# Optimization experiments

Measured on AMD Instinct MI355X. Metric: run time of the kernel, lower is better.

Reference implementation:

```python
import jax, jax.numpy as jnp
from jax import lax
import numpy as np

H = 16        # hidden_size == input_size
L = 8         # num_layers


def _lstm_layer(x_seq, Wih, Whh, bih, bhh):
    # x_seq: [B, T, H] -> outputs [B, T, H]; PyTorch gate order i,f,g,o
    B = x_seq.shape[0]
    b = bih + bhh  # [4H]

    def step(carry, xt):
        h, c = carry
        gates = xt @ Wih.T + h @ Whh.T + b  # [B, 4H]
        i, f, g, o = jnp.split(gates, 4, axis=-1)
        c = jax.nn.sigmoid(f) * c + jax.nn.sigmoid(i) * jnp.tanh(g)
        h = jax.nn.sigmoid(o) * jnp.tanh(c)
        return (h, c), h

    h0 = jnp.zeros((B, H), x_seq.dtype)
    (_, _), hs = lax.scan(step, (h0, h0), jnp.swapaxes(x_seq, 0, 1))
    return jnp.swapaxes(hs, 0, 1)  # [B, T, H]


def setup_inputs() -> dict:
    key = jax.random.key(0)
    ks = jax.random.split(key, 9)
    s = 1.0 / np.sqrt(H)  # PyTorch default init scale
    x = jax.random.normal(ks[0], (2048, 512, H), dtype=jnp.float32)
    W_ih = jax.random.uniform(ks[1], (L, 4 * H, H), jnp.float32, -s, s)
    W_hh = jax.random.uniform(ks[2], (L, 4 * H, H), jnp.float32, -s, s)
    b_ih = jax.random.uniform(ks[3], (L, 4 * H), jnp.float32, -s, s)
    b_hh = jax.random.uniform(ks[4], (L, 4 * H), jnp.float32, -s, s)
    Wp = jax.random.uniform(ks[5], (3, H), jnp.float32, -s, s)
    bp = jax.random.uniform(ks[6], (3,), jnp.float32, -s, s)
    Wo = jax.random.uniform(ks[7], (3, H), jnp.float32, -s, s)
    bo = jax.random.uniform(ks[8], (3,), jnp.float32, -s, s)
    return {"x": x, "W_ih": W_ih, "W_hh": W_hh, "b_ih": b_ih, "b_hh": b_hh,
            "Wp": Wp, "bp": bp, "Wo": Wo, "bo": bo}


def reference(x, W_ih, W_hh, b_ih, b_hh, Wp, bp, Wo, bo):
    h = x
    for l in range(L):  # fixed small layer count
        h = _lstm_layer(h, W_ih[l], W_hh[l], b_ih[l], b_hh[l])
    last = h[:, -1, :]                       # [B, H]
    position = last @ Wp.T + bp              # [B, 3]
    orientation = jnp.tanh(last @ Wo.T + bo) # [B, 3]
    return jnp.concatenate((position, orientation), axis=1)  # [B, 6]
```

## Files before the change

kernel.cpp:

```cpp
#include <hip/hip_runtime.h>
#include <math.h>

typedef _Float16 f16x8 __attribute__((ext_vector_type(8)));
typedef float    f32x4 __attribute__((ext_vector_type(4)));

constexpr int kT    = 512;
constexpr int kH    = 16;
constexpr int kL    = 8;
constexpr int kG    = 64;
constexpr int kNB   = 8;
constexpr int kPad  = 24;
constexpr int kRows = 9;
constexpr int kSlots= 16;
constexpr int kLyr  = kL + 1;
constexpr int kSE   = kLyr * kRows * kPad;
constexpr int kIters= 33;

constexpr float kL2E = 1.4426950408889634f;

__device__ __forceinline__ float sigm2(float z) {
    return __builtin_amdgcn_rcpf(1.0f + __builtin_amdgcn_exp2f(z));
}
__device__ __forceinline__ void cbar() { asm volatile("" ::: "memory"); }

__global__ __launch_bounds__(512, 2)
void lstm_rp(const float* __restrict__ x,
             const float* __restrict__ Wih, const float* __restrict__ Whh,
             const float* __restrict__ bih, const float* __restrict__ bhh,
             const float* __restrict__ Wp,  const float* __restrict__ bpos,
             const float* __restrict__ Wo,  const float* __restrict__ bori,
             float* __restrict__ out)
{
    const int tid  = threadIdx.x;
    const int l    = tid >> 6;
    const int lane = tid & 63;
    const int n    = lane & 15;
    const int q    = lane >> 4;
    const int bn   = n & 7;
    const bool cLow = (n < 8);
    const bool bact = ((q >> 1) == (n >> 3));

    __shared__ __align__(16) _Float16 hb[kSlots][kLyr][kRows][kPad];
    __shared__ int cnt[kL];

    {
        int* hz = (int*)&hb[0][0][0][0];
        for (int i = tid; i < (int)(sizeof(hb) / 4); i += 512) hz[i] = 0;
        if (tid < kL) cnt[tid] = -1;
    }

    auto loadA = [&](const float* W, int tile) -> f16x8 {
        const int unit = tile + (n >> 2) + ((q >= 2) ? 4 : 0);
        const int row  = (n & 3) * 16 + unit;
        const float* src = W + (size_t)l * kG * kH + row * kH + (q & 1) * 8;
        f16x8 a;
        #pragma unroll
        for (int j = 0; j < 8; ++j) a[j] = (_Float16)src[j];
        return a;
    };
    const f16x8 A1P1 = loadA(Wih, 0), A2P1 = loadA(Whh, 0);
    const f16x8 A1P2 = loadA(Wih, 8), A2P2 = loadA(Whh, 8);

    const int u1 = (cLow ? q : 4 + q);
    float ab1[4], ab2[4];
    #pragma unroll
    for (int r = 0; r < 4; ++r) {
        const float sc = (r == 2) ? (-2.0f * kL2E) : (-kL2E);
        const int g1 = l * kG + r * 16 + u1;
        const int g2 = l * kG + r * 16 + u1 + 8;
        ab1[r] = sc * (bih[g1] + bhh[g1]);
        ab2[r] = sc * (bih[g2] + bhh[g2]);
    }

    const int boff = (bact ? bn * kPad : 8 * kPad) + (q & 1) * 8;
    const _Float16* b1b = &hb[0][l    ][0][0] + boff;
    const _Float16* b2b = &hb[0][l + 1][0][0] + boff;
    _Float16* hw1 = &hb[0][l + 1][bn][u1];
    _Float16* hw2 = &hb[0][l + 1][bn][u1 + 8];
    _Float16* xwb = &hb[0][0][lane >> 3][(lane & 7) * 2];

    const float* xg_ptr =
        x + ((size_t)(blockIdx.x * kNB + (lane >> 3)) * kT) * kH + (lane & 7) * 2;
    float xg0 = 0.f, xg1 = 0.f;
    if (l == 0) {
        float2 v0 = *(const float2*)(xg_ptr);
        hb[15][0][lane >> 3][(lane & 7) * 2]     = (_Float16)v0.x;
        hb[15][0][lane >> 3][(lane & 7) * 2 + 1] = (_Float16)v0.y;
        float2 v1 = *(const float2*)(xg_ptr + kH);
        xg0 = v1.x; xg1 = v1.y;
    }

    float c1 = 0.f, c2 = 0.f;
    __syncthreads();

    const f32x4 zeroC = {0.f, 0.f, 0.f, 0.f};
    volatile const int* upc = (l > 0)      ? &cnt[l - 1] : nullptr;
    volatile const int* dnc = (l < kL - 1) ? &cnt[l + 1] : nullptr;

    for (int it = 0; it < kIters; ++it) {
        const int sb = it * 16;
        #pragma unroll
        for (int k = 0; k < 16; ++k) {
            const int s = sb + k;

            if ((k & 1) == 0 && l > 0) {
                while (*upc < s) __builtin_amdgcn_s_sleep(1);
                cbar();
            }
            if ((k == 0 || k == 8) && l < kL - 1) {
                const int need = (k == 0) ? (sb - 8) : sb;
                while (*dnc < need) __builtin_amdgcn_s_sleep(1);
                cbar();
            }

            const int  t      = s - l;
            const bool active = ((unsigned)t < (unsigned)kT);
            const int  rs     = (k + 15) & 15;
            const int  roff   = rs * kSE;
            const int  woff   = k * kSE;

            const f16x8 B1 = *(const f16x8*)(b1b + roff);
            const f16x8 B2 = *(const f16x8*)(b2b + roff);

            f32x4 d1 = __builtin_amdgcn_mfma_f32_16x16x32_f16(A2P1, B2, zeroC, 0, 0, 0);
            f32x4 d2 = __builtin_amdgcn_mfma_f32_16x16x32_f16(A2P2, B2, zeroC, 0, 0, 0);
            d1 = __builtin_amdgcn_mfma_f32_16x16x32_f16(A1P1, B1, d1, 0, 0, 0);
            d2 = __builtin_amdgcn_mfma_f32_16x16x32_f16(A1P2, B1, d2, 0, 0, 0);

            {
                const float iv = sigm2(fmaf(-kL2E,        d1[0], ab1[0]));
                const float fv = sigm2(fmaf(-kL2E,        d1[1], ab1[1]));
                const float gv = fmaf(2.f, sigm2(fmaf(-2.f * kL2E, d1[2], ab1[2])), -1.f);
                const float ov = sigm2(fmaf(-kL2E,        d1[3], ab1[3]));
                float cn = fmaf(fv, c1, iv * gv);
                cn = active ? cn : 0.0f;
                c1 = cn;
                const float tc = fmaf(2.f, sigm2(-2.f * kL2E * cn), -1.f);
                hw1[woff] = (_Float16)(ov * tc);
            }
            {
                const float iv = sigm2(fmaf(-kL2E,        d2[0], ab2[0]));
                const float fv = sigm2(fmaf(-kL2E,        d2[1], ab2[1]));
                const float gv = fmaf(2.f, sigm2(fmaf(-2.f * kL2E, d2[2], ab2[2])), -1.f);
                const float ov = sigm2(fmaf(-kL2E,        d2[3], ab2[3]));
                float cn = fmaf(fv, c2, iv * gv);
                cn = active ? cn : 0.0f;
                c2 = cn;
                const float tc = fmaf(2.f, sigm2(-2.f * kL2E * cn), -1.f);
                hw2[woff] = (_Float16)(ov * tc);
            }

            if (l == 0) {
                _Float16* xw = xwb + woff;
                xw[0] = (_Float16)xg0;
                xw[1] = (_Float16)xg1;
                int tn = s + 2; if (tn > kT - 1) tn = kT - 1;
                float2 v = *(const float2*)(xg_ptr + (size_t)tn * kH);
                xg0 = v.x; xg1 = v.y;
            }

            if (k & 1) {
                cbar();
                if (lane == 0) *(volatile int*)&cnt[l] = s;
            }
        }
    }

    __syncthreads();

    if (l == kL - 1) {
        const int bb = lane >> 3;
        const int r  = lane & 7;
        if (r < 6) {
            const bool  isP   = (r < 3);
            const float* wrow = isP ? (Wp + r * kH) : (Wo + (r - 3) * kH);
            float acc = isP ? bpos[r] : bori[r - 3];
            #pragma unroll
            for (int u = 0; u < kH; ++u)
                acc = fmaf((float)hb[6][kL][bb][u], wrow[u], acc);
            if (!isP) acc = fmaf(2.f, sigm2(-2.f * kL2E * acc), -1.f);
            out[(size_t)(blockIdx.x * kNB + bb) * 6 + r] = acc;
        }
    }
}

extern "C" void kernel_launch(void* const* d_in, const int* in_sizes, int n_in,
                              void* d_out, int out_size, void* d_ws, size_t ws_size,
                              hipStream_t stream) {
    const float* x    = (const float*)d_in[0];
    const float* Wih  = (const float*)d_in[1];
    const float* Whh  = (const float*)d_in[2];
    const float* bih  = (const float*)d_in[3];
    const float* bhh  = (const float*)d_in[4];
    const float* Wp   = (const float*)d_in[5];
    const float* bpos = (const float*)d_in[6];
    const float* Wo   = (const float*)d_in[7];
    const float* bori = (const float*)d_in[8];
    float* out = (float*)d_out;

    const int B = in_sizes[0] / (kT * kH);
    lstm_rp<<<dim3(B / kNB), dim3(512), 0, stream>>>(x, Wih, Whh, bih, bhh,
                                                     Wp, bpos, Wo, bori, out);
}
```

Baseline: 312.8 us.

## Software-pipeline input-projection MFMA one step ahead and fold gate scaling into weights

The input-to-hidden MFMA for the next timestep is now issued at the end of each step, with the bias as its accumulator, so only the recurrent MFMA sits on the critical path each step. The exp2 scale factors are folded into the f16 weights, and both hidden units per lane are interleaved so they go out as a single packed f16x2 store. Ring-buffer slot indexing and the upstream wait condition shift by one step to match. Pre-scaling the weights before the f16 conversion changes rounding, and the tighter dependency distance needs the up-layer to run one step ahead.

```diff
diff --git a/kernel.cpp b/kernel.cpp
--- a/kernel.cpp
+++ b/kernel.cpp
@@ -2,6 +2,7 @@
 #include <math.h>
 
 typedef _Float16 f16x8 __attribute__((ext_vector_type(8)));
+typedef _Float16 f16x2 __attribute__((ext_vector_type(2)));
 typedef float    f32x4 __attribute__((ext_vector_type(4)));
 
 constexpr int kT    = 512;
@@ -15,16 +16,16 @@
 constexpr int kLyr  = kL + 1;
 constexpr int kSE   = kLyr * kRows * kPad;
 constexpr int kIters= 33;
+constexpr int kLastS= kIters * 16 - 1;
 
 constexpr float kL2E = 1.4426950408889634f;
 
-__device__ __forceinline__ float sigm2(float z) {
-    return __builtin_amdgcn_rcpf(1.0f + __builtin_amdgcn_exp2f(z));
-}
-__device__ __forceinline__ void cbar() { asm volatile("" ::: "memory"); }
+__device__ __forceinline__ float ex2(float w)  { return __builtin_amdgcn_exp2f(w); }
+__device__ __forceinline__ float rcp1p(float e){ return __builtin_amdgcn_rcpf(1.0f + e); }
+__device__ __forceinline__ void  cbar()        { asm volatile("" ::: "memory"); }
 
 __global__ __launch_bounds__(512, 2)
-void lstm_rp(const float* __restrict__ x,
+void lstm_sp(const float* __restrict__ x,
              const float* __restrict__ Wih, const float* __restrict__ Whh,
              const float* __restrict__ bih, const float* __restrict__ bhh,
              const float* __restrict__ Wp,  const float* __restrict__ bpos,
@@ -37,7 +38,6 @@
     const int n    = lane & 15;
     const int q    = lane >> 4;
     const int bn   = n & 7;
-    const bool cLow = (n < 8);
     const bool bact = ((q >> 1) == (n >> 3));
 
     __shared__ __align__(16) _Float16 hb[kSlots][kLyr][kRows][kPad];
@@ -48,55 +48,68 @@
         for (int i = tid; i < (int)(sizeof(hb) / 4); i += 512) hz[i] = 0;
         if (tid < kL) cnt[tid] = -1;
     }
-
-    auto loadA = [&](const float* W, int tile) -> f16x8 {
-        const int unit = tile + (n >> 2) + ((q >= 2) ? 4 : 0);
-        const int row  = (n & 3) * 16 + unit;
-        const float* src = W + (size_t)l * kG * kH + row * kH + (q & 1) * 8;
+    __syncthreads();
+
+    const float asc = ((n & 3) == 2) ? (-2.0f * kL2E) : (-kL2E);
+    auto loadA = [&](const float* W, int T) -> f16x8 {
+        const int wrow = (n & 3) * 16 + (n >> 2) + 4 * (q >> 1) + 8 * T;
+        const float* src = W + (size_t)l * kG * kH + wrow * kH;
         f16x8 a;
         #pragma unroll
-        for (int j = 0; j < 8; ++j) a[j] = (_Float16)src[j];
+        for (int j = 0; j < 8; ++j) {
+            const int u = (q & 1) * 4 + (j >> 1) + 8 * (j & 1);
+            a[j] = (_Float16)(asc * src[u]);
+        }
         return a;
     };
-    const f16x8 A1P1 = loadA(Wih, 0), A2P1 = loadA(Whh, 0);
-    const f16x8 A1P2 = loadA(Wih, 8), A2P2 = loadA(Whh, 8);
-
-    const int u1 = (cLow ? q : 4 + q);
-    float ab1[4], ab2[4];
+    const f16x8 A1T0 = loadA(Wih, 0), A2T0 = loadA(Whh, 0);
+    const f16x8 A1T1 = loadA(Wih, 1), A2T1 = loadA(Whh, 1);
+
+    const int u0 = q + 4 * (n >> 3);
+    f32x4 bias0, bias1;
     #pragma unroll
     for (int r = 0; r < 4; ++r) {
         const float sc = (r == 2) ? (-2.0f * kL2E) : (-kL2E);
-        const int g1 = l * kG + r * 16 + u1;
-        const int g2 = l * kG + r * 16 + u1 + 8;
-        ab1[r] = sc * (bih[g1] + bhh[g1]);
-        ab2[r] = sc * (bih[g2] + bhh[g2]);
+        const int g0 = l * kG + r * 16 + u0;
+        bias0[r] = sc * (bih[g0] + bhh[g0]);
+        bias1[r] = sc * (bih[g0 + 8] + bhh[g0 + 8]);
     }
 
     const int boff = (bact ? bn * kPad : 8 * kPad) + (q & 1) * 8;
     const _Float16* b1b = &hb[0][l    ][0][0] + boff;
     const _Float16* b2b = &hb[0][l + 1][0][0] + boff;
-    _Float16* hw1 = &hb[0][l + 1][bn][u1];
-    _Float16* hw2 = &hb[0][l + 1][bn][u1 + 8];
-    _Float16* xwb = &hb[0][0][lane >> 3][(lane & 7) * 2];
-
+    _Float16* hw  = &hb[0][l + 1][bn][2 * u0];
+    _Float16* xw  = &hb[0][0][lane >> 3][2 * (lane & 7)];
+
+    const int xa = lane & 7;
     const float* xg_ptr =
-        x + ((size_t)(blockIdx.x * kNB + (lane >> 3)) * kT) * kH + (lane & 7) * 2;
+        x + ((size_t)(blockIdx.x * kNB + (lane >> 3)) * kT) * kH;
     float xg0 = 0.f, xg1 = 0.f;
     if (l == 0) {
-        float2 v0 = *(const float2*)(xg_ptr);
-        hb[15][0][lane >> 3][(lane & 7) * 2]     = (_Float16)v0.x;
-        hb[15][0][lane >> 3][(lane & 7) * 2 + 1] = (_Float16)v0.y;
-        float2 v1 = *(const float2*)(xg_ptr + kH);
-        xg0 = v1.x; xg1 = v1.y;
-    }
-
-    float c1 = 0.f, c2 = 0.f;
-    __syncthreads();
-
-    const f32x4 zeroC = {0.f, 0.f, 0.f, 0.f};
+        #pragma unroll
+        for (int t = 0; t < 2; ++t) {
+            f16x2 xp = { (_Float16)xg_ptr[t * kH + xa],
+                         (_Float16)xg_ptr[t * kH + xa + 8] };
+            *(f16x2*)(xw + t * kSE) = xp;
+        }
+        xg0 = xg_ptr[2 * kH + xa];
+        xg1 = xg_ptr[2 * kH + xa + 8];
+    }
+
+    f16x8 B2r = *(const f16x8*)(b2b);
+    {
+        const f16x8 B1p = *(const f16x8*)(b1b);
+    }
+    const f16x8 B1p = *(const f16x8*)(b1b);
+    f32x4 dIn0 = __builtin_amdgcn_mfma_f32_16x16x32_f16(A1T0, B1p, bias0, 0, 0, 0);
+    f32x4 dIn1 = __builtin_amdgcn_mfma_f32_16x16x32_f16(A1T1, B1p, bias1, 0, 0, 0);
+
+    float c0 = 0.f, c1 = 0.f;
+
     volatile const int* upc = (l > 0)      ? &cnt[l - 1] : nullptr;
     volatile const int* dnc = (l < kL - 1) ? &cnt[l + 1] : nullptr;
 
+    #pragma unroll 1
     for (int it = 0; it < kIters; ++it) {
         const int sb = it * 16;
         #pragma unroll
@@ -104,7 +117,8 @@
             const int s = sb + k;
 
             if ((k & 1) == 0 && l > 0) {
-                while (*upc < s) __builtin_amdgcn_s_sleep(1);
+                int need = s + 1; if (need > kLastS) need = kLastS;
+                while (*upc < need) __builtin_amdgcn_s_sleep(1);
                 cbar();
             }
             if ((k == 0 || k == 8) && l < kL - 1) {
@@ -113,51 +127,54 @@
                 cbar();
             }
 
-            const int  t      = s - l;
-            const bool active = ((unsigned)t < (unsigned)kT);
-            const int  rs     = (k + 15) & 15;
-            const int  roff   = rs * kSE;
-            const int  woff   = k * kSE;
-
-            const f16x8 B1 = *(const f16x8*)(b1b + roff);
-            const f16x8 B2 = *(const f16x8*)(b2b + roff);
-
-            f32x4 d1 = __builtin_amdgcn_mfma_f32_16x16x32_f16(A2P1, B2, zeroC, 0, 0, 0);
-            f32x4 d2 = __builtin_amdgcn_mfma_f32_16x16x32_f16(A2P2, B2, zeroC, 0, 0, 0);
-            d1 = __builtin_amdgcn_mfma_f32_16x16x32_f16(A1P1, B1, d1, 0, 0, 0);
-            d2 = __builtin_amdgcn_mfma_f32_16x16x32_f16(A1P2, B1, d2, 0, 0, 0);
-
+            const int  slot1  = ((k + 1) & 15) * kSE;
+            const int  slot2  = ((k + 2) & 15) * kSE;
+            const bool active = ((unsigned)(s - l) < (unsigned)kT);
+
+            const f16x8 B1n = *(const f16x8*)(b1b + slot1);
+
+            f32x4 d0 = __builtin_amdgcn_mfma_f32_16x16x32_f16(A2T0, B2r, dIn0, 0, 0, 0);
+            f32x4 d1 = __builtin_amdgcn_mfma_f32_16x16x32_f16(A2T1, B2r, dIn1, 0, 0, 0);
+
+            float h0, h1;
             {
-                const float iv = sigm2(fmaf(-kL2E,        d1[0], ab1[0]));
-                const float fv = sigm2(fmaf(-kL2E,        d1[1], ab1[1]));
-                const float gv = fmaf(2.f, sigm2(fmaf(-2.f * kL2E, d1[2], ab1[2])), -1.f);
-                const float ov = sigm2(fmaf(-kL2E,        d1[3], ab1[3]));
-                float cn = fmaf(fv, c1, iv * gv);
+                const float si = rcp1p(ex2(d0[0]));
+                const float sf = rcp1p(ex2(d0[1]));
+                const float sg = rcp1p(ex2(d0[2]));
+                const float so = rcp1p(ex2(d0[3]));
+                const float tgp = fmaf(-4.0f * kL2E, sg, 2.0f * kL2E);
+                float cn = fmaf(sf, c0, si * tgp);
+                cn = active ? cn : 0.0f;
+                c0 = cn;
+                h0 = so * fmaf(2.0f, rcp1p(ex2(cn)), -1.0f);
+            }
+            {
+                const float si = rcp1p(ex2(d1[0]));
+                const float sf = rcp1p(ex2(d1[1]));
+                const float sg = rcp1p(ex2(d1[2]));
+                const float so = rcp1p(ex2(d1[3]));
+                const float tgp = fmaf(-4.0f * kL2E, sg, 2.0f * kL2E);
+                float cn = fmaf(sf, c1, si * tgp);
                 cn = active ? cn : 0.0f;
                 c1 = cn;
-                const float tc = fmaf(2.f, sigm2(-2.f * kL2E * cn), -1.f);
-                hw1[woff] = (_Float16)(ov * tc);
-            }
-            {
-                const float iv = sigm2(fmaf(-kL2E,        d2[0], ab2[0]));
-                const float fv = sigm2(fmaf(-kL2E,        d2[1], ab2[1]));
-                const float gv = fmaf(2.f, sigm2(fmaf(-2.f * kL2E, d2[2], ab2[2])), -1.f);
-                const float ov = sigm2(fmaf(-kL2E,        d2[3], ab2[3]));
-                float cn = fmaf(fv, c2, iv * gv);
-                cn = active ? cn : 0.0f;
-                c2 = cn;
-                const float tc = fmaf(2.f, sigm2(-2.f * kL2E * cn), -1.f);
-                hw2[woff] = (_Float16)(ov * tc);
-            }
+                h1 = so * fmaf(2.0f, rcp1p(ex2(cn)), -1.0f);
+            }
+
+            f16x2 hp = { (_Float16)h0, (_Float16)h1 };
+            *(f16x2*)(hw + slot1) = hp;
 
             if (l == 0) {
-                _Float16* xw = xwb + woff;
-                xw[0] = (_Float16)xg0;
-                xw[1] = (_Float16)xg1;
-                int tn = s + 2; if (tn > kT - 1) tn = kT - 1;
-                float2 v = *(const float2*)(xg_ptr + (size_t)tn * kH);
-                xg0 = v.x; xg1 = v.y;
-            }
+                f16x2 xp = { (_Float16)xg0, (_Float16)xg1 };
+                *(f16x2*)(xw + slot2) = xp;
+                int tn = s + 3; if (tn > kT - 1) tn = kT - 1;
+                xg0 = xg_ptr[(size_t)tn * kH + xa];
+                xg1 = xg_ptr[(size_t)tn * kH + xa + 8];
+            }
+
+            B2r = *(const f16x8*)(b2b + slot1);
+
+            dIn0 = __builtin_amdgcn_mfma_f32_16x16x32_f16(A1T0, B1n, bias0, 0, 0, 0);
+            dIn1 = __builtin_amdgcn_mfma_f32_16x16x32_f16(A1T1, B1n, bias1, 0, 0, 0);
 
             if (k & 1) {
                 cbar();
@@ -176,9 +193,11 @@
             const float* wrow = isP ? (Wp + r * kH) : (Wo + (r - 3) * kH);
             float acc = isP ? bpos[r] : bori[r - 3];
             #pragma unroll
-            for (int u = 0; u < kH; ++u)
-                acc = fmaf((float)hb[6][kL][bb][u], wrow[u], acc);
-            if (!isP) acc = fmaf(2.f, sigm2(-2.f * kL2E * acc), -1.f);
+            for (int u = 0; u < kH; ++u) {
+                const int p = 2 * (u & 7) + (u >> 3);
+                acc = fmaf((float)hb[7][kL][bb][p], wrow[u], acc);
+            }
+            if (!isP) acc = fmaf(2.0f, rcp1p(ex2(-2.0f * kL2E * acc)), -1.0f);
             out[(size_t)(blockIdx.x * kNB + bb) * 6 + r] = acc;
         }
     }
@@ -199,6 +218,6 @@
     float* out = (float*)d_out;
 
     const int B = in_sizes[0] / (kT * kH);
-    lstm_rp<<<dim3(B / kNB), dim3(512), 0, stream>>>(x, Wih, Whh, bih, bhh,
+    lstm_sp<<<dim3(B / kNB), dim3(512), 0, stream>>>(x, Wih, Whh, bih, bhh,
                                                      Wp, bpos, Wo, bori, out);
 }
```

Result: faster. 300.1 us (-4.1%).
